# Performance work log

Hardware: AMD Instinct MI355X
Metric: run time of the kernel (lower is better)

The kernel has to match this reference:

```python
import jax, jax.numpy as jnp
import numpy as np

K = 1024
DIM = 64
DECAY = 0.99
EPS = 1e-05
CC = 0.25


def setup_inputs() -> dict:
    key = jax.random.key(0)
    k1, k2 = jax.random.split(key)
    inputs = jax.random.normal(k1, (32, DIM, 64, 64), dtype=jnp.float32)
    # embedding initialized uniform(-1/K, 1/K); ema_w starts as a copy
    emb_w = jax.random.uniform(k2, (K, DIM), dtype=jnp.float32, minval=-1.0 / K, maxval=1.0 / K)
    ema_w = emb_w
    ema_cluster_size = jnp.zeros((K,), dtype=jnp.float32)
    return {"inputs": inputs, "emb_w": emb_w, "ema_cluster_size": ema_cluster_size, "ema_w": ema_w}


def reference(inputs, emb_w, ema_cluster_size, ema_w):
    # NCHW -> NHWC
    x = jnp.transpose(inputs, (0, 2, 3, 1))  # [B,H,W,D]
    B, H, W, D = x.shape
    flat = x.reshape(-1, D)  # [N,D]
    # squared L2 distances: |f|^2 - 2 f.W^T + |w|^2
    d = (jnp.sum(flat * flat, axis=1, keepdims=True)
         - 2.0 * flat @ emb_w.T
         + jnp.sum(emb_w * emb_w, axis=1)[None, :])  # [N,K]
    idx = jnp.argmin(d, axis=1)  # [N]
    encodings = idx.reshape(B, H, W)
    quantized = emb_w[idx].reshape(B, H, W, D)

    # training-mode EMA update (matches one_hot.sum(0) and one_hot.T @ flatten)
    counts = jax.ops.segment_sum(jnp.ones_like(idx, dtype=jnp.float32), idx, num_segments=K)
    new_cs = ema_cluster_size * DECAY + (1.0 - DECAY) * counts
    n = jnp.sum(new_cs)
    new_cs = (new_cs + EPS) / (n + K * EPS) * n
    dw = jax.ops.segment_sum(flat, idx, num_segments=K)  # [K,D]
    new_ema_w = ema_w * DECAY + (1.0 - DECAY) * dw
    new_emb_w = new_ema_w / new_cs[:, None]

    e_latent_loss = jnp.mean((quantized - x) ** 2)  # both terms equal in value
    loss = e_latent_loss + CC * e_latent_loss
    # straight-through (value-equal in fwd)
    q_out = jnp.transpose(quantized, (0, 3, 1, 2))  # NHWC -> NCHW
    nll = jnp.ones((1,), dtype=jnp.float32)
    return q_out, encodings, loss, nll, new_cs, new_ema_w, new_emb_w
```

## Files before the change

kernel.cpp:

```cpp
#include <hip/hip_runtime.h>
#include <math.h>

#define KCODES 1024
#define DIMV   64
#define NROWS  131072
#define HWSZ   4096
#define NELEM  8388608
#define CAP    224
#define CANDCAP 1024
#define RPB    128


typedef __attribute__((ext_vector_type(8))) short bf16x8;
typedef __attribute__((ext_vector_type(4))) float f32x4;

static __device__ __forceinline__ unsigned short f2bf(float x) {
    unsigned int u = __float_as_uint(x);
    unsigned int r = (u + 0x7FFFu + ((u >> 16) & 1u)) >> 16;
    return (unsigned short)r;
}

__global__ __launch_bounds__(64) void vq_prep3_kernel(
    const float* __restrict__ emb, float* __restrict__ s_w,
    unsigned short* __restrict__ WB, unsigned int* __restrict__ wmax_bits)
{
    int k = blockIdx.x, t = threadIdx.x;
    float v = emb[k * DIMV + t];

    {
        int cg = k >> 4, n = k & 15;
        int kh = t >> 5, q = (t & 31) >> 3, j = t & 7;
        WB[((cg * 2 + kh) * 4 + q) * 128 + n * 8 + j] = f2bf(v);
    }

    float av = fabsf(v);
    #pragma unroll
    for (int off = 32; off > 0; off >>= 1)
        av = fmaxf(av, __shfl_down(av, off, 64));
    if (t == 0) atomicMax(wmax_bits, __float_as_uint(av));

    __shared__ float sv[64];
    __shared__ float sr[8];
    sv[t] = v;
    __syncthreads();
    if (t < 8) {
        float x = sv[t];
        float sq = x * x;
        asm("" : "+v"(sq));
        float r = sq;
        #pragma unroll
        for (int m = 1; m < 8; ++m) {
            float y = sv[8 * m + t];
            float s2 = y * y;
            asm("" : "+v"(s2));
            r += s2;
        }
        sr[t] = r;
    }
    __syncthreads();
    if (t == 0)
        s_w[k] = ((sr[0] + sr[1]) + (sr[2] + sr[3])) + ((sr[4] + sr[5]) + (sr[6] + sr[7]));
}

__global__ __launch_bounds__(256, 3) void vq_assign_kernel(
    const float* __restrict__ inp, const float* __restrict__ emb,
    const unsigned short* __restrict__ WB, const float* __restrict__ s_w,
    const unsigned int* __restrict__ wmax_bits,
    float* __restrict__ tmp_flat, float* __restrict__ enc_out,
    double* __restrict__ loss_sum, int* __restrict__ counts,
    int* __restrict__ rowlist)
{
    __shared__ float At[RPB * 65];
    __shared__ float sWL[KCODES];
    __shared__ float sfL[RPB];
    __shared__ float errL[RPB];
    __shared__ float thL[RPB];
    __shared__ float wred[RPB * 4];
    __shared__ unsigned long long rowBest[RPB];
    __shared__ int bkL[RPB];
    __shared__ int candL[CANDCAP];
    __shared__ int candCnt;

    const int t = threadIdx.x;
    const int n0 = blockIdx.x * RPB;
    const int bq  = n0 >> 12;
    const int hw0 = n0 & 4095;
    const float* fin = inp + (size_t)bq * (DIMV * HWSZ) + hw0;

    if (t < RPB) rowBest[t] = ~0ULL;
    if (t == 0) candCnt = 0;

    #pragma unroll
    for (int j = 0; j < 4; ++j) sWL[j * 256 + t] = s_w[j * 256 + t];

    #pragma unroll
    for (int j = 0; j < 8; ++j) {
        int id = j * 256 + t;
        int i = id >> 5;
        int c4 = id & 31;
        float4 v = *(const float4*)(fin + (size_t)i * HWSZ + 4 * c4);
        int r = 4 * c4;
        At[(r + 0) * 65 + i] = v.x + v.x;  At[(r + 1) * 65 + i] = v.y + v.y;
        At[(r + 2) * 65 + i] = v.z + v.z;  At[(r + 3) * 65 + i] = v.w + v.w;
    }
    __syncthreads();

    if (t < RPB) {
        const float* gr = &At[t * 65];
        float r8[8];
        #pragma unroll
        for (int j = 0; j < 8; ++j) {
            float h = 0.5f * gr[j];
            float sq = h * h;
            asm("" : "+v"(sq));
            r8[j] = sq;
        }
        #pragma unroll
        for (int m = 1; m < 8; ++m) {
            #pragma unroll
            for (int j = 0; j < 8; ++j) {
                float h = 0.5f * gr[8 * m + j];
                float sq = h * h;
                asm("" : "+v"(sq));
                r8[j] += sq;
            }
        }
        sfL[t] = ((r8[0] + r8[1]) + (r8[2] + r8[3])) + ((r8[4] + r8[5]) + (r8[6] + r8[7]));
        float S = 0.0f;
        #pragma unroll
        for (int i = 0; i < 64; ++i) S += fabsf(gr[i]);
        float wmax = __uint_as_float(*wmax_bits);
        errL[t] = fmaf(S * wmax, 0.015625f, 2e-5f);
    }
    __syncthreads();

    const int wv = t >> 6, l = t & 63;
    const int m = l & 15, q = l >> 4;
    bf16x8 afr[8][2];
    #pragma unroll
    for (int rg = 0; rg < 8; ++rg) {
        int row = rg * 16 + m;
        const float* gr = &At[row * 65];
        #pragma unroll
        for (int kh = 0; kh < 2; ++kh) {
            bf16x8 a;
            #pragma unroll
            for (int j = 0; j < 8; ++j)
                a[j] = (short)f2bf(gr[kh * 32 + q * 8 + j]);
            afr[rg][kh] = a;
        }
    }

    const unsigned short* wbw = WB + (wv * 16) * 1024 + q * 128 + m * 8;
    const int swb0 = wv * 256 + m;

    float mn[8][4];
    #pragma unroll
    for (int rg = 0; rg < 8; ++rg)
        #pragma unroll
        for (int reg = 0; reg < 4; ++reg) mn[rg][reg] = 3.0e38f;

    {
        bf16x8 pa0 = *(const bf16x8*)(wbw);
        bf16x8 pa1 = *(const bf16x8*)(wbw + 512);
        float   swa = sWL[swb0];
        bf16x8 pb0 = *(const bf16x8*)(wbw + 1024);
        bf16x8 pb1 = *(const bf16x8*)(wbw + 1024 + 512);
        float   swb = sWL[swb0 + 16];
        for (int cg = 0; cg < 16; cg += 2) {
            #pragma unroll
            for (int rg = 0; rg < 8; ++rg) {
                f32x4 acc = {0.f, 0.f, 0.f, 0.f};
                acc = __builtin_amdgcn_mfma_f32_16x16x32_bf16(afr[rg][0], pa0, acc, 0, 0, 0);
                acc = __builtin_amdgcn_mfma_f32_16x16x32_bf16(afr[rg][1], pa1, acc, 0, 0, 0);
                #pragma unroll
                for (int reg = 0; reg < 4; ++reg)
                    mn[rg][reg] = fminf(mn[rg][reg], swa - acc[reg]);
            }
            {
                int cn = (cg + 2) & 15;
                pa0 = *(const bf16x8*)(wbw + cn * 1024);
                pa1 = *(const bf16x8*)(wbw + cn * 1024 + 512);
                swa = sWL[swb0 + cn * 16];
            }
            #pragma unroll
            for (int rg = 0; rg < 8; ++rg) {
                f32x4 acc = {0.f, 0.f, 0.f, 0.f};
                acc = __builtin_amdgcn_mfma_f32_16x16x32_bf16(afr[rg][0], pb0, acc, 0, 0, 0);
                acc = __builtin_amdgcn_mfma_f32_16x16x32_bf16(afr[rg][1], pb1, acc, 0, 0, 0);
                #pragma unroll
                for (int reg = 0; reg < 4; ++reg)
                    mn[rg][reg] = fminf(mn[rg][reg], swb - acc[reg]);
            }
            {
                int cn = (cg + 3) & 15;
                pb0 = *(const bf16x8*)(wbw + cn * 1024);
                pb1 = *(const bf16x8*)(wbw + cn * 1024 + 512);
                swb = sWL[swb0 + cn * 16];
            }
        }
    }

    #pragma unroll
    for (int rg = 0; rg < 8; ++rg)
        #pragma unroll
        for (int reg = 0; reg < 4; ++reg) {
            float v = mn[rg][reg];
            v = fminf(v, __shfl_xor(v, 1, 64));
            v = fminf(v, __shfl_xor(v, 2, 64));
            v = fminf(v, __shfl_xor(v, 4, 64));
            v = fminf(v, __shfl_xor(v, 8, 64));
            mn[rg][reg] = v;
        }
    if (m == 0) {
        #pragma unroll
        for (int rg = 0; rg < 8; ++rg)
            #pragma unroll
            for (int reg = 0; reg < 4; ++reg)
                wred[(rg * 16 + q * 4 + reg) * 4 + wv] = mn[rg][reg];
    }
    __syncthreads();
    if (t < RPB)
        thL[t] = fminf(fminf(wred[t * 4 + 0], wred[t * 4 + 1]),
                       fminf(wred[t * 4 + 2], wred[t * 4 + 3])) + errL[t];
    __syncthreads();

    float th[8][4];
    #pragma unroll
    for (int rg = 0; rg < 8; ++rg)
        #pragma unroll
        for (int reg = 0; reg < 4; ++reg)
            th[rg][reg] = thL[rg * 16 + q * 4 + reg];

    {
        bf16x8 pa0 = *(const bf16x8*)(wbw);
        bf16x8 pa1 = *(const bf16x8*)(wbw + 512);
        float   swa = sWL[swb0];
        bf16x8 pb0 = *(const bf16x8*)(wbw + 1024);
        bf16x8 pb1 = *(const bf16x8*)(wbw + 1024 + 512);
        float   swb = sWL[swb0 + 16];
        for (int cg = 0; cg < 16; cg += 2) {
            #pragma unroll
            for (int rg = 0; rg < 8; ++rg) {
                f32x4 acc = {0.f, 0.f, 0.f, 0.f};
                acc = __builtin_amdgcn_mfma_f32_16x16x32_bf16(afr[rg][0], pa0, acc, 0, 0, 0);
                acc = __builtin_amdgcn_mfma_f32_16x16x32_bf16(afr[rg][1], pa1, acc, 0, 0, 0);
                #pragma unroll
                for (int reg = 0; reg < 4; ++reg) {
                    if (swa - acc[reg] <= th[rg][reg]) {
                        int row = rg * 16 + q * 4 + reg;
                        int p = atomicAdd(&candCnt, 1);
                        if (p < CANDCAP) candL[p] = (row << 10) | (wv * 256 + cg * 16 + m);
                    }
                }
            }
            {
                int cn = (cg + 2) & 15;
                pa0 = *(const bf16x8*)(wbw + cn * 1024);
                pa1 = *(const bf16x8*)(wbw + cn * 1024 + 512);
                swa = sWL[swb0 + cn * 16];
            }
            #pragma unroll
            for (int rg = 0; rg < 8; ++rg) {
                f32x4 acc = {0.f, 0.f, 0.f, 0.f};
                acc = __builtin_amdgcn_mfma_f32_16x16x32_bf16(afr[rg][0], pb0, acc, 0, 0, 0);
                acc = __builtin_amdgcn_mfma_f32_16x16x32_bf16(afr[rg][1], pb1, acc, 0, 0, 0);
                #pragma unroll
                for (int reg = 0; reg < 4; ++reg) {
                    if (swb - acc[reg] <= th[rg][reg]) {
                        int row = rg * 16 + q * 4 + reg;
                        int p = atomicAdd(&candCnt, 1);
                        if (p < CANDCAP) candL[p] = (row << 10) | (wv * 256 + (cg + 1) * 16 + m);
                    }
                }
            }
            {
                int cn = (cg + 3) & 15;
                pb0 = *(const bf16x8*)(wbw + cn * 1024);
                pb1 = *(const bf16x8*)(wbw + cn * 1024 + 512);
                swb = sWL[swb0 + cn * 16];
            }
        }
    }
    __syncthreads();

    int nc = candCnt < CANDCAP ? candCnt : CANDCAP;
    for (int c = t; c < nc; c += 256) {
        int pk = candL[c];
        int r = pk >> 10, k = pk & 1023;
        const float* wk = emb + (size_t)k * DIMV;
        const float* gr = &At[r * 65];
        float acc = 0.0f;
        #pragma unroll
        for (int i = 0; i < DIMV; ++i)
            acc = __builtin_fmaf(gr[i], wk[i], acc);
        float d = (sfL[r] - acc) + sWL[k];
        unsigned int u = __float_as_uint(d);
        unsigned int s = (u & 0x80000000u) ? ~u : (u | 0x80000000u);
        unsigned long long key = ((unsigned long long)s << 32) | (unsigned int)k;
        atomicMin(&rowBest[r], key);
    }
    __syncthreads();

    if (t < RPB && (rowBest[t] == ~0ULL || candCnt > CANDCAP)) {
        int r = t;
        const float* gr = &At[r * 65];
        float bd = 3.0e38f; int bk = 0;
        for (int k = 0; k < KCODES; ++k) {
            const float* wk = emb + (size_t)k * DIMV;
            float acc = 0.0f;
            #pragma unroll
            for (int i = 0; i < DIMV; ++i)
                acc = __builtin_fmaf(gr[i], wk[i], acc);
            float d = (sfL[r] - acc) + sWL[k];
            if (d < bd) { bd = d; bk = k; }
        }
        unsigned int u = __float_as_uint(bd);
        unsigned int s = (u & 0x80000000u) ? ~u : (u | 0x80000000u);
        rowBest[r] = ((unsigned long long)s << 32) | (unsigned int)bk;
    }
    __syncthreads();

    if (t < RPB) {
        int r = t;
        int bk = (int)(rowBest[r] & 1023ULL);
        enc_out[n0 + r] = (float)bk;
        bkL[r] = bk;
        int pos = atomicAdd(&counts[bk], 1);
        if (pos < CAP) rowlist[bk * CAP + pos] = n0 + r;
    }
    __syncthreads();

    float* tq = tmp_flat + (size_t)n0 * DIMV;
    double lsum = 0.0;
    #pragma unroll
    for (int j = 0; j < 32; ++j) {
        int idx = j * 256 + t;
        int r = idx >> 6;
        int i = idx & 63;
        int bk = bkL[r];
        float fi = 0.5f * At[r * 65 + i];
        tq[r * DIMV + i] = fi;
        float qv = emb[bk * DIMV + i];
        double dq = (double)qv - (double)fi;
        lsum = fma(dq, dq, lsum);
    }
    #pragma unroll
    for (int off = 32; off > 0; off >>= 1)
        lsum += __shfl_down(lsum, off, 64);
    if ((t & 63) == 0) atomicAdd(loss_sum, lsum);
}

__global__ __launch_bounds__(256) void vq_dw_all_kernel(
    const float* __restrict__ tmp_flat, const int* __restrict__ rowlist,
    const int* __restrict__ counts, const float* __restrict__ ema_cs,
    const float* __restrict__ ema_w, const double* __restrict__ loss_sum,
    float* __restrict__ out_loss, float* __restrict__ out_nll,
    float* __restrict__ out_ncs, float* __restrict__ out_nema,
    float* __restrict__ out_nemb)
{
    const int k = blockIdx.x;
    const int t = threadIdx.x;
    const double DECAY = 0.99;
    const double OMD   = 1.0 - 0.99;
    const double EPSV  = 1e-5;

    __shared__ double sm[256];
    double part = 0.0;
    #pragma unroll
    for (int j0 = 0; j0 < 4; ++j0) {
        int j = j0 * 256 + t;
        part += (double)ema_cs[j] * DECAY + OMD * (double)counts[j];
    }
    sm[t] = part;
    __syncthreads();
    #pragma unroll
    for (int off = 128; off > 0; off >>= 1) {
        if (t < off) sm[t] += sm[t + off];
        __syncthreads();
    }
    double nsum = sm[0];

    int cnt = counts[k];
    double ncs = (double)ema_cs[k] * DECAY + OMD * (double)cnt;
    double adj = (ncs + EPSV) / (nsum + (double)KCODES * EPSV) * nsum;
    if (t == 0) out_ncs[k] = (float)adj;
    if (k == 0 && t == 0) {
        double e = loss_sum[0] / (double)NELEM;
        out_loss[0] = (float)(e + 0.25 * e);
        out_nll[0]  = 1.0f;
    }

    int i = t & 63;
    int sub = t >> 6;
    int cap = cnt < CAP ? cnt : CAP;

    float acc = 0.0f;
    #pragma unroll 4
    for (int r = sub; r < cap; r += 4) {
        int n = rowlist[k * CAP + r];
        acc += tmp_flat[(size_t)n * DIMV + i];
    }

    __shared__ float red[256];
    red[t] = acc;
    __syncthreads();
    if (t < 128) red[t] += red[t + 128];
    __syncthreads();
    if (t < 64) {
        float dwv = red[t] + red[t + 64];
        int idx = k * DIMV + i;
        double ne = (double)ema_w[idx] * DECAY + OMD * (double)dwv;
        out_nema[idx] = (float)ne;
        out_nemb[idx] = (float)(ne / adj);
    }
}

__global__ __launch_bounds__(256) void vq_qout_kernel(
    const float* __restrict__ enc, const float* __restrict__ emb,
    float* __restrict__ q_out)
{
    __shared__ int bkL[128];
    const int t = threadIdx.x;
    const int n0 = blockIdx.x * 128;
    const int bq  = n0 >> 12;
    const int hw0 = n0 & 4095;
    if (t < 128) bkL[t] = (int)enc[n0 + t];
    __syncthreads();
    float* qo = q_out + (size_t)bq * (DIMV * HWSZ) + hw0;
    #pragma unroll
    for (int j = 0; j < 32; ++j) {
        int idx = j * 256 + t;
        int r = idx & 127;
        int i = idx >> 7;
        qo[(size_t)i * HWSZ + r] = emb[bkL[r] * DIMV + i];
    }
}

extern "C" void kernel_launch(void* const* d_in, const int* in_sizes, int n_in,
                              void* d_out, int out_size, void* d_ws, size_t ws_size,
                              hipStream_t stream) {
    const float* inp    = (const float*)d_in[0];
    const float* emb    = (const float*)d_in[1];
    const float* ema_cs = (const float*)d_in[2];
    const float* ema_w  = (const float*)d_in[3];

    char* ws = (char*)d_ws;
    double*         loss_sum  = (double*)(ws + 0);
    unsigned int*   wmax_bits = (unsigned int*)(ws + 16);
    int*            counts    = (int*)(ws + 32);
    float*          s_w       = (float*)(ws + 4128);
    unsigned short* WB        = (unsigned short*)(ws + 8224);
    int*            rowlist   = (int*)(ws + 139296);

    float* out       = (float*)d_out;
    float* q_out     = out;
    float* enc_out   = out + 8388608;
    float* out_loss  = out + 8519680;
    float* out_nll   = out + 8519681;
    float* out_ncs   = out + 8519682;
    float* out_nema  = out + 8520706;
    float* out_nemb  = out + 8586242;

    hipMemsetAsync(ws, 0, 4128, stream);
    hipLaunchKernelGGL(vq_prep3_kernel, dim3(KCODES), dim3(64), 0, stream,
                       emb, s_w, WB, wmax_bits);
    hipLaunchKernelGGL(vq_assign_kernel, dim3(NROWS / RPB), dim3(256), 0, stream,
                       inp, emb, WB, s_w, wmax_bits,
                       q_out , enc_out, loss_sum, counts, rowlist);
    hipLaunchKernelGGL(vq_dw_all_kernel, dim3(KCODES), dim3(256), 0, stream,
                       q_out , rowlist, counts, ema_cs, ema_w, loss_sum,
                       out_loss, out_nll, out_ncs, out_nema, out_nemb);
    hipLaunchKernelGGL(vq_qout_kernel, dim3(NROWS / 128), dim3(256), 0, stream,
                       enc_out, emb, q_out);
}
```

Measured before the change: 255.3 us.

## Replace second MFMA candidate pass with per-lane group minima and exact fp32 rescoring

Removes the second full bf16 MFMA sweep over all codes. Candidate selection now uses each lane's running minimum over its 16-code group: a whole group becomes a candidate when that minimum is within the threshold. Each candidate group is then rescored exactly in fp32 across its 16 codes, four at a time, with a single atomicMin per group. The shared s_w copy is dropped in favour of global reads, and the wred and candL buffers share one LDS pool, which lowers shared-memory use. In exchange, each candidate now costs about 16 fp32 dot products instead of one, and overflow of CANDCAP may become more frequent, which sends rows to the slow brute-force fallback.

```diff
diff --git a/kernel.cpp b/kernel.cpp
--- a/kernel.cpp
+++ b/kernel.cpp
@@ -18,6 +18,12 @@
     unsigned int u = __float_as_uint(x);
     unsigned int r = (u + 0x7FFFu + ((u >> 16) & 1u)) >> 16;
     return (unsigned short)r;
+}
+
+static __device__ __forceinline__ unsigned long long dkey(float d, int k) {
+    unsigned int u = __float_as_uint(d);
+    unsigned int s = (u & 0x80000000u) ? ~u : (u | 0x80000000u);
+    return ((unsigned long long)s << 32) | (unsigned int)k;
 }
 
 __global__ __launch_bounds__(64) void vq_prep3_kernel(
@@ -71,14 +77,12 @@
     int* __restrict__ rowlist)
 {
     __shared__ float At[RPB * 65];
-    __shared__ float sWL[KCODES];
     __shared__ float sfL[RPB];
     __shared__ float errL[RPB];
     __shared__ float thL[RPB];
-    __shared__ float wred[RPB * 4];
     __shared__ unsigned long long rowBest[RPB];
     __shared__ int bkL[RPB];
-    __shared__ int candL[CANDCAP];
+    __shared__ int shpool[CANDCAP];
     __shared__ int candCnt;
 
     const int t = threadIdx.x;
@@ -89,9 +93,6 @@
 
     if (t < RPB) rowBest[t] = ~0ULL;
     if (t == 0) candCnt = 0;
-
-    #pragma unroll
-    for (int j = 0; j < 4; ++j) sWL[j * 256 + t] = s_w[j * 256 + t];
 
     #pragma unroll
     for (int j = 0; j < 8; ++j) {
@@ -152,7 +153,7 @@
     }
 
     const unsigned short* wbw = WB + (wv * 16) * 1024 + q * 128 + m * 8;
-    const int swb0 = wv * 256 + m;
+    const float* swm = s_w + wv * 256 + m;
 
     float mn[8][4];
     #pragma unroll
@@ -163,10 +164,10 @@
     {
         bf16x8 pa0 = *(const bf16x8*)(wbw);
         bf16x8 pa1 = *(const bf16x8*)(wbw + 512);
-        float   swa = sWL[swb0];
+        float   swa = swm[0];
         bf16x8 pb0 = *(const bf16x8*)(wbw + 1024);
         bf16x8 pb1 = *(const bf16x8*)(wbw + 1024 + 512);
-        float   swb = sWL[swb0 + 16];
+        float   swb = swm[16];
         for (int cg = 0; cg < 16; cg += 2) {
             #pragma unroll
             for (int rg = 0; rg < 8; ++rg) {
@@ -181,7 +182,7 @@
                 int cn = (cg + 2) & 15;
                 pa0 = *(const bf16x8*)(wbw + cn * 1024);
                 pa1 = *(const bf16x8*)(wbw + cn * 1024 + 512);
-                swa = sWL[swb0 + cn * 16];
+                swa = swm[cn * 16];
             }
             #pragma unroll
             for (int rg = 0; rg < 8; ++rg) {
@@ -196,11 +197,12 @@
                 int cn = (cg + 3) & 15;
                 pb0 = *(const bf16x8*)(wbw + cn * 1024);
                 pb1 = *(const bf16x8*)(wbw + cn * 1024 + 512);
-                swb = sWL[swb0 + cn * 16];
-            }
-        }
-    }
-
+                swb = swm[cn * 16];
+            }
+        }
+    }
+
+    float* wred = (float*)shpool;
     #pragma unroll
     for (int rg = 0; rg < 8; ++rg)
         #pragma unroll
@@ -210,95 +212,65 @@
             v = fminf(v, __shfl_xor(v, 2, 64));
             v = fminf(v, __shfl_xor(v, 4, 64));
             v = fminf(v, __shfl_xor(v, 8, 64));
-            mn[rg][reg] = v;
-        }
-    if (m == 0) {
-        #pragma unroll
-        for (int rg = 0; rg < 8; ++rg)
-            #pragma unroll
-            for (int reg = 0; reg < 4; ++reg)
-                wred[(rg * 16 + q * 4 + reg) * 4 + wv] = mn[rg][reg];
-    }
+            if (m == 0) wred[(rg * 16 + q * 4 + reg) * 4 + wv] = v;
+        }
     __syncthreads();
     if (t < RPB)
         thL[t] = fminf(fminf(wred[t * 4 + 0], wred[t * 4 + 1]),
                        fminf(wred[t * 4 + 2], wred[t * 4 + 3])) + errL[t];
     __syncthreads();
 
-    float th[8][4];
+    int* candL = shpool;
     #pragma unroll
     for (int rg = 0; rg < 8; ++rg)
         #pragma unroll
-        for (int reg = 0; reg < 4; ++reg)
-            th[rg][reg] = thL[rg * 16 + q * 4 + reg];
-
-    {
-        bf16x8 pa0 = *(const bf16x8*)(wbw);
-        bf16x8 pa1 = *(const bf16x8*)(wbw + 512);
-        float   swa = sWL[swb0];
-        bf16x8 pb0 = *(const bf16x8*)(wbw + 1024);
-        bf16x8 pb1 = *(const bf16x8*)(wbw + 1024 + 512);
-        float   swb = sWL[swb0 + 16];
-        for (int cg = 0; cg < 16; cg += 2) {
-            #pragma unroll
-            for (int rg = 0; rg < 8; ++rg) {
-                f32x4 acc = {0.f, 0.f, 0.f, 0.f};
-                acc = __builtin_amdgcn_mfma_f32_16x16x32_bf16(afr[rg][0], pa0, acc, 0, 0, 0);
-                acc = __builtin_amdgcn_mfma_f32_16x16x32_bf16(afr[rg][1], pa1, acc, 0, 0, 0);
-                #pragma unroll
-                for (int reg = 0; reg < 4; ++reg) {
-                    if (swa - acc[reg] <= th[rg][reg]) {
-                        int row = rg * 16 + q * 4 + reg;
-                        int p = atomicAdd(&candCnt, 1);
-                        if (p < CANDCAP) candL[p] = (row << 10) | (wv * 256 + cg * 16 + m);
-                    }
-                }
-            }
-            {
-                int cn = (cg + 2) & 15;
-                pa0 = *(const bf16x8*)(wbw + cn * 1024);
-                pa1 = *(const bf16x8*)(wbw + cn * 1024 + 512);
-                swa = sWL[swb0 + cn * 16];
-            }
-            #pragma unroll
-            for (int rg = 0; rg < 8; ++rg) {
-                f32x4 acc = {0.f, 0.f, 0.f, 0.f};
-                acc = __builtin_amdgcn_mfma_f32_16x16x32_bf16(afr[rg][0], pb0, acc, 0, 0, 0);
-                acc = __builtin_amdgcn_mfma_f32_16x16x32_bf16(afr[rg][1], pb1, acc, 0, 0, 0);
-                #pragma unroll
-                for (int reg = 0; reg < 4; ++reg) {
-                    if (swb - acc[reg] <= th[rg][reg]) {
-                        int row = rg * 16 + q * 4 + reg;
-                        int p = atomicAdd(&candCnt, 1);
-                        if (p < CANDCAP) candL[p] = (row << 10) | (wv * 256 + (cg + 1) * 16 + m);
-                    }
-                }
-            }
-            {
-                int cn = (cg + 3) & 15;
-                pb0 = *(const bf16x8*)(wbw + cn * 1024);
-                pb1 = *(const bf16x8*)(wbw + cn * 1024 + 512);
-                swb = sWL[swb0 + cn * 16];
-            }
-        }
-    }
-    __syncthreads();
-
-    int nc = candCnt < CANDCAP ? candCnt : CANDCAP;
-    for (int c = t; c < nc; c += 256) {
+        for (int reg = 0; reg < 4; ++reg) {
+            if (mn[rg][reg] <= thL[rg * 16 + q * 4 + reg]) {
+                int p = atomicAdd(&candCnt, 1);
+                if (p < CANDCAP)
+                    candL[p] = ((rg * 16 + q * 4 + reg) << 6) | (wv * 16 + m);
+            }
+        }
+    __syncthreads();
+
+    int ng = candCnt < CANDCAP ? candCnt : CANDCAP;
+    for (int c = t; c < ng; c += 256) {
         int pk = candL[c];
-        int r = pk >> 10, k = pk & 1023;
-        const float* wk = emb + (size_t)k * DIMV;
+        int r = pk >> 6;
+        int g6 = pk & 63;
+        int gbase = (g6 >> 4) * 256 + (g6 & 15);
         const float* gr = &At[r * 65];
-        float acc = 0.0f;
-        #pragma unroll
-        for (int i = 0; i < DIMV; ++i)
-            acc = __builtin_fmaf(gr[i], wk[i], acc);
-        float d = (sfL[r] - acc) + sWL[k];
-        unsigned int u = __float_as_uint(d);
-        unsigned int s = (u & 0x80000000u) ? ~u : (u | 0x80000000u);
-        unsigned long long key = ((unsigned long long)s << 32) | (unsigned int)k;
-        atomicMin(&rowBest[r], key);
+        float sf = sfL[r];
+        unsigned long long best = ~0ULL;
+        #pragma unroll 1
+        for (int cb = 0; cb < 16; cb += 4) {
+            int k0 = gbase + (cb + 0) * 16;
+            int k1 = gbase + (cb + 1) * 16;
+            int k2 = gbase + (cb + 2) * 16;
+            int k3 = gbase + (cb + 3) * 16;
+            const float* w0 = emb + (size_t)k0 * DIMV;
+            const float* w1 = emb + (size_t)k1 * DIMV;
+            const float* w2 = emb + (size_t)k2 * DIMV;
+            const float* w3 = emb + (size_t)k3 * DIMV;
+            float a0 = 0.f, a1 = 0.f, a2 = 0.f, a3 = 0.f;
+            #pragma unroll
+            for (int i = 0; i < DIMV; ++i) {
+                float g = gr[i];
+                a0 = __builtin_fmaf(g, w0[i], a0);
+                a1 = __builtin_fmaf(g, w1[i], a1);
+                a2 = __builtin_fmaf(g, w2[i], a2);
+                a3 = __builtin_fmaf(g, w3[i], a3);
+            }
+            unsigned long long c0 = dkey((sf - a0) + s_w[k0], k0);
+            unsigned long long c1 = dkey((sf - a1) + s_w[k1], k1);
+            unsigned long long c2 = dkey((sf - a2) + s_w[k2], k2);
+            unsigned long long c3 = dkey((sf - a3) + s_w[k3], k3);
+            unsigned long long m01 = c0 < c1 ? c0 : c1;
+            unsigned long long m23 = c2 < c3 ? c2 : c3;
+            unsigned long long mm = m01 < m23 ? m01 : m23;
+            if (mm < best) best = mm;
+        }
+        atomicMin(&rowBest[r], best);
     }
     __syncthreads();
 
@@ -312,12 +284,10 @@
             #pragma unroll
             for (int i = 0; i < DIMV; ++i)
                 acc = __builtin_fmaf(gr[i], wk[i], acc);
-            float d = (sfL[r] - acc) + sWL[k];
+            float d = (sfL[r] - acc) + s_w[k];
             if (d < bd) { bd = d; bk = k; }
         }
-        unsigned int u = __float_as_uint(bd);
-        unsigned int s = (u & 0x80000000u) ? ~u : (u | 0x80000000u);
-        rowBest[r] = ((unsigned long long)s << 32) | (unsigned int)bk;
+        rowBest[r] = dkey(bd, bk);
     }
     __syncthreads();
 
```

After: 797.8 us. 213% more time.
